# Kernel optimization log

Measured on AMD Instinct MI355X. Metric: run time of the kernel, lower is better.

Reference implementation:

```python
import jax, jax.numpy as jnp
import numpy as np

EPS = 1e-5

def layer_norm(x, g, b):
    mu = jnp.mean(x, axis=-1, keepdims=True)
    var = jnp.var(x, axis=-1, keepdims=True)
    return (x - mu) * jax.lax.rsqrt(var + EPS) * g + b

def setup_inputs() -> dict:
    key = jax.random.key(0)
    ks = jax.random.split(key, 8)
    B, N, C, H = 4, 1024, 1024, 16
    Dh = C * 4
    std = 0.02
    return {
        "x": jax.random.normal(ks[0], (B, N, C), dtype=jnp.float32),
        "qkv_w": jax.random.normal(ks[1], (3 * C, C), dtype=jnp.float32) * std,
        "proj_w": jax.random.normal(ks[2], (C, C), dtype=jnp.float32) * std,
        "proj_b": jnp.zeros((C,), dtype=jnp.float32),
        "fc1_w": jax.random.normal(ks[3], (Dh, C), dtype=jnp.float32) * std,
        "fc1_b": jnp.zeros((Dh,), dtype=jnp.float32),
        "fc2_w": jax.random.normal(ks[4], (C, Dh), dtype=jnp.float32) * std,
        "fc2_b": jnp.zeros((C,), dtype=jnp.float32),
        "ln1_g": jnp.ones((C,), dtype=jnp.float32),
        "ln1_b": jnp.zeros((C,), dtype=jnp.float32),
        "ln2_g": jnp.ones((C,), dtype=jnp.float32),
        "ln2_b": jnp.zeros((C,), dtype=jnp.float32),
        "lnh_g": jnp.ones((Dh,), dtype=jnp.float32),
        "lnh_b": jnp.zeros((Dh,), dtype=jnp.float32),
    }

def reference(x, qkv_w, proj_w, proj_b, fc1_w, fc1_b, fc2_w, fc2_b,
              ln1_g, ln1_b, ln2_g, ln2_b, lnh_g, lnh_b):
    B, N, C = x.shape
    H = 16
    Dh = C // H
    scale = Dh ** (-0.5)

    # --- attention sublayer (pre-norm) ---
    h = layer_norm(x, ln1_g, ln1_b)
    qkv = (h @ qkv_w.T).reshape(B, N, 3, H, Dh).transpose(2, 0, 3, 1, 4)  # [3,B,H,N,Dh]
    q, k, v = qkv[0], qkv[1], qkv[2]
    attn = jnp.einsum('bhid,bhjd->bhij', q, k) * scale
    attn = jax.nn.softmax(attn, axis=-1)
    o = jnp.einsum('bhij,bhjd->bhid', attn, v)          # [B,H,N,Dh]
    o = o.transpose(0, 2, 1, 3).reshape(B, N, C)
    o = o @ proj_w.T + proj_b
    x = x + o

    # --- MLP sublayer (pre-norm, with LN on hidden per use_ln=True) ---
    h = layer_norm(x, ln2_g, ln2_b)
    u = jax.nn.gelu(h @ fc1_w.T + fc1_b, approximate=False)  # torch nn.GELU = erf form
    u = layer_norm(u, lnh_g, lnh_b)
    m = u @ fc2_w.T + fc2_b
    return x + m
```

## Files before the change

### kernel.cpp

```cpp
#include <hip/hip_runtime.h>
#include <hip/hip_bf16.h>
#include <math.h>


#define TOKENS 4096
#define CDIM   1024
#define HEADS  16
#define DHEAD  64
#define HID    4096

typedef __attribute__((ext_vector_type(4))) float  floatx4;
typedef __attribute__((ext_vector_type(8))) short  short8;

__global__ __launch_bounds__(256) void cvt_all(
    const float* __restrict__ s0, const float* __restrict__ s1,
    const float* __restrict__ s2, const float* __restrict__ s3,
    __hip_bfloat16* __restrict__ dst)
{
    long i = (long)blockIdx.x * 256 + threadIdx.x;
    const float* src;
    long base;
    if (i < 768l * 1024)       { src = s0; base = 0; }
    else if (i < 1792l * 1024) { src = s1; base = 768l * 1024; }
    else if (i < 2816l * 1024) { src = s2; base = 1792l * 1024; }
    else                       { src = s3; base = 2816l * 1024; }
    float4 v = ((const float4*)src)[i - base];
    __hip_bfloat16 t[4];
    t[0] = __float2bfloat16(v.x);
    t[1] = __float2bfloat16(v.y);
    t[2] = __float2bfloat16(v.z);
    t[3] = __float2bfloat16(v.w);
    *(uint2*)(dst + 4l * i) = *(uint2*)t;
}

__global__ __launch_bounds__(256) void ln_f32_kernel(
    const float* __restrict__ x, const float* __restrict__ g,
    const float* __restrict__ b, __hip_bfloat16* __restrict__ y, int C)
{
    int row = blockIdx.x;
    const float* xr = x + (long)row * C;
    __hip_bfloat16* yr = y + (long)row * C;

    float s = 0.f, ss = 0.f;
    for (int i = threadIdx.x; i < C; i += 256) {
        float v = xr[i];
        s += v; ss += v * v;
    }
    #pragma unroll
    for (int d = 32; d; d >>= 1) {
        s  += __shfl_down(s, d);
        ss += __shfl_down(ss, d);
    }
    __shared__ float buf[4][2];
    int wid = threadIdx.x >> 6, lane = threadIdx.x & 63;
    if (lane == 0) { buf[wid][0] = s; buf[wid][1] = ss; }
    __syncthreads();
    if (threadIdx.x == 0) {
        s = buf[0][0] + buf[1][0] + buf[2][0] + buf[3][0];
        ss = buf[0][1] + buf[1][1] + buf[2][1] + buf[3][1];
        buf[0][0] = s; buf[0][1] = ss;
    }
    __syncthreads();
    s = buf[0][0]; ss = buf[0][1];

    float invC = 1.f / (float)C;
    float mu = s * invC;
    float var = ss * invC - mu * mu;
    float inv = rsqrtf(var + 1e-5f);
    for (int i = threadIdx.x; i < C; i += 256) {
        yr[i] = __float2bfloat16((xr[i] - mu) * inv * g[i] + b[i]);
    }
}

__global__ __launch_bounds__(256) void ln_bf16_kernel(
    const __hip_bfloat16* __restrict__ x, const float* __restrict__ g,
    const float* __restrict__ b, __hip_bfloat16* __restrict__ y, int C)
{
    int row = blockIdx.x;
    const __hip_bfloat16* xr = x + (long)row * C;
    __hip_bfloat16* yr = y + (long)row * C;

    float s = 0.f, ss = 0.f;
    for (int i = threadIdx.x; i < C; i += 256) {
        float v = __bfloat162float(xr[i]);
        s += v; ss += v * v;
    }
    #pragma unroll
    for (int d = 32; d; d >>= 1) {
        s  += __shfl_down(s, d);
        ss += __shfl_down(ss, d);
    }
    __shared__ float buf[4][2];
    int wid = threadIdx.x >> 6, lane = threadIdx.x & 63;
    if (lane == 0) { buf[wid][0] = s; buf[wid][1] = ss; }
    __syncthreads();
    if (threadIdx.x == 0) {
        s = buf[0][0] + buf[1][0] + buf[2][0] + buf[3][0];
        ss = buf[0][1] + buf[1][1] + buf[2][1] + buf[3][1];
        buf[0][0] = s; buf[0][1] = ss;
    }
    __syncthreads();
    s = buf[0][0]; ss = buf[0][1];

    float invC = 1.f / (float)C;
    float mu = s * invC;
    float var = ss * invC - mu * mu;
    float inv = rsqrtf(var + 1e-5f);
    for (int i = threadIdx.x; i < C; i += 256) {
        float v = __bfloat162float(xr[i]);
        yr[i] = __float2bfloat16((v - mu) * inv * g[i] + b[i]);
    }
}

template <int TN>
__global__ __launch_bounds__(256, 3) void gemm_mfma(
    const __hip_bfloat16* __restrict__ A,
    const __hip_bfloat16* __restrict__ W,
    const float* __restrict__ bias, const float* __restrict__ residual,
    void* __restrict__ Cout, int M, int N, int K, int act, int out_bf16)
{
    constexpr int WN = (TN == 128) ? 2 : 1;
    constexpr int WM = 4 / WN;
    constexpr int FJ = 4;
    constexpr int FI = 128 / (WM * 16);

    __shared__ __hip_bfloat16 Asl[2][128 * 32];
    __shared__ __hip_bfloat16 Bsl[2][TN * 32];

    int tid = threadIdx.x;
    int wave = tid >> 6, lane = tid & 63;

    int mt, nt;
    {
        int gx = gridDim.x, gy = gridDim.y;
        int lin = blockIdx.y * gx + blockIdx.x;
        if ((gy & 7) == 0) {
            int chunk = gy >> 3;
            int xcd = lin & 7, q = lin >> 3;
            mt = xcd * chunk + (q % chunk);
            nt = q / chunk;
        } else { mt = blockIdx.y; nt = blockIdx.x; }
    }
    int bm = mt * 128, bn = nt * TN;
    int wm = wave & (WM - 1), wn = wave / WM;
    int fm = lane & 15, quad = lane >> 4;

    int srow = lane >> 2;
    int skk  = (lane & 3) * 8;

    const __hip_bfloat16* Ap = A + (long)(bm + wave * 16 + srow) * K + skk;
    const __hip_bfloat16* Bp = W + (long)(bn + wave * 16 + srow) * K + skk;
    const long a64 = (long)64 * K;

    const int nk = K / 32;
    floatx4 acc[FI][FJ] = {};
    const int aoff = (wave * 16 + srow) * 32 + skk;

    uint4 a0A, a1A, b0A, b1A;
    uint4 a0B, a1B, b0B, b1B;

#define GLOADA(t) { const long o = (long)(t) * 32; \
    a0A = *(const uint4*)(Ap + o); a1A = *(const uint4*)(Ap + a64 + o); \
    b0A = *(const uint4*)(Bp + o); if (TN == 128) b1A = *(const uint4*)(Bp + a64 + o); }
#define GLOADB(t) { const long o = (long)(t) * 32; \
    a0B = *(const uint4*)(Ap + o); a1B = *(const uint4*)(Ap + a64 + o); \
    b0B = *(const uint4*)(Bp + o); if (TN == 128) b1B = *(const uint4*)(Bp + a64 + o); }
#define LWRITEA(bf) { *(uint4*)&Asl[bf][aoff] = a0A; *(uint4*)&Asl[bf][aoff + 2048] = a1A; \
    *(uint4*)&Bsl[bf][aoff] = b0A; if (TN == 128) *(uint4*)&Bsl[bf][aoff + 2048] = b1A; }
#define LWRITEB(bf) { *(uint4*)&Asl[bf][aoff] = a0B; *(uint4*)&Asl[bf][aoff + 2048] = a1B; \
    *(uint4*)&Bsl[bf][aoff] = b0B; if (TN == 128) *(uint4*)&Bsl[bf][aoff + 2048] = b1B; }

    auto compute = [&](int buf) {
        const __hip_bfloat16* Ab = Asl[buf];
        const __hip_bfloat16* Bb = Bsl[buf];
        short8 bfr[FJ];
        #pragma unroll
        for (int j = 0; j < FJ; ++j)
            bfr[j] = *(const short8*)(Bb + (wn * 64 + j * 16 + fm) * 32 + quad * 8);
        #pragma unroll
        for (int i = 0; i < FI; ++i) {
            short8 af = *(const short8*)(Ab + (wm * FI * 16 + i * 16 + fm) * 32 + quad * 8);
            #pragma unroll
            for (int j = 0; j < FJ; ++j)
                acc[i][j] = __builtin_amdgcn_mfma_f32_16x16x32_bf16(
                    af, bfr[j], acc[i][j], 0, 0, 0);
        }
    };

    GLOADA(0); GLOADB(1);
    LWRITEA(0);
    GLOADA(2);
    __syncthreads();

    for (int kt = 0; kt < nk; kt += 2) {
        compute(0);
        LWRITEB(1);
        if (kt + 3 < nk) GLOADB(kt + 3);
        __syncthreads();
        compute(1);
        if (kt + 2 < nk) {
            LWRITEA(0);
            if (kt + 4 < nk) GLOADA(kt + 4);
        }
        __syncthreads();
    }
#undef GLOADA
#undef GLOADB
#undef LWRITEA
#undef LWRITEB

    int mbase = bm + wm * FI * 16;
    int nbase = bn + wn * 64;
    #pragma unroll
    for (int i = 0; i < FI; ++i) {
        #pragma unroll
        for (int j = 0; j < FJ; ++j) {
            int ncol = nbase + j * 16 + fm;
            #pragma unroll
            for (int r = 0; r < 4; ++r) {
                int mrow = mbase + i * 16 + quad * 4 + r;
                float v = acc[i][j][r];
                if (bias) v += bias[ncol];
                if (act == 1) v = 0.5f * v * (1.f + erff(v * 0.70710678118654752f));
                if (residual) v += residual[(long)mrow * N + ncol];
                if (out_bf16)
                    ((__hip_bfloat16*)Cout)[(long)mrow * N + ncol] = __float2bfloat16(v);
                else
                    ((float*)Cout)[(long)mrow * N + ncol] = v;
            }
        }
    }
}

__global__ __launch_bounds__(256) void attn_mfma(
    const __hip_bfloat16* __restrict__ qkv, __hip_bfloat16* __restrict__ o_out)
{
    __shared__ __align__(16) char Ks[2][64 * 144];
    __shared__ __align__(16) char Vt[2][64 * 144];
    __shared__ __align__(16) char Ps[4 * 16 * 144];

    const int C3 = 3 * CDIM;
    int lin = blockIdx.x;
    int xcd = lin & 7, q = lin >> 3;
    int bh = xcd * 8 + (q >> 4);
    int qt = q & 15;
    int b = bh >> 4, hh = bh & 15;
    int tid = threadIdx.x, wave = tid >> 6, lane = tid & 63;
    int l = lane & 15, quad = lane >> 4;

    const __hip_bfloat16* qrow =
        qkv + (long)(b * 1024 + qt * 64 + wave * 16 + l) * C3 + hh * DHEAD;
    short8 qf0 = *(const short8*)(qrow + quad * 8);
    short8 qf1 = *(const short8*)(qrow + 32 + quad * 8);

    char* Psw = Ps + wave * (16 * 144);

    int sc = tid & 7;
    int skl = tid >> 3;

    const __hip_bfloat16* Kbase = qkv + (long)(b * 1024) * C3 + CDIM + hh * DHEAD;
    const __hip_bfloat16* Vbase = qkv + (long)(b * 1024) * C3 + 2 * CDIM + hh * DHEAD;
    const int kpp = skl ^ (sc << 2);

    floatx4 facc[4] = {};
    float mrun = -1e30f, lrun = 0.f;

    uint4 kA0, kA1, vA0, vA1;
    uint4 kB0, kB1, vB0, vB1;

#define GKV(t, k0, k1, v0, v1) { \
    const __hip_bfloat16* Kg = Kbase + (long)((t) * 64) * C3; \
    const __hip_bfloat16* Vg = Vbase + (long)((t) * 64) * C3; \
    k0 = *(const uint4*)(Kg + (long)skl * C3 + sc * 8); \
    k1 = *(const uint4*)(Kg + (long)(skl + 32) * C3 + sc * 8); \
    v0 = *(const uint4*)(Vg + (long)(2 * skl) * C3 + sc * 8); \
    v1 = *(const uint4*)(Vg + (long)(2 * skl + 1) * C3 + sc * 8); }
#define WKV(bf, k0, k1, v0, v1) { \
    *(uint4*)(Ks[bf] + skl * 144 + sc * 16) = k0; \
    *(uint4*)(Ks[bf] + (skl + 32) * 144 + sc * 16) = k1; \
    const ushort* e0 = (const ushort*)&v0; \
    const ushort* e1 = (const ushort*)&v1; \
    _Pragma("unroll") \
    for (int j = 0; j < 8; ++j) { \
        unsigned dw = (unsigned)e0[j] | ((unsigned)e1[j] << 16); \
        *(unsigned*)(Vt[bf] + (sc * 8 + j) * 144 + kpp * 4) = dw; \
    } }

    auto compute = [&](int buf) {
        floatx4 st[4] = {};
        #pragma unroll
        for (int kb = 0; kb < 4; ++kb) {
            short8 k0 = *(const short8*)(Ks[buf] + (kb * 16 + l) * 144 + quad * 16);
            short8 k1 = *(const short8*)(Ks[buf] + (kb * 16 + l) * 144 + 64 + quad * 16);
            st[kb] = __builtin_amdgcn_mfma_f32_16x16x32_bf16(k0, qf0, st[kb], 0, 0, 0);
            st[kb] = __builtin_amdgcn_mfma_f32_16x16x32_bf16(k1, qf1, st[kb], 0, 0, 0);
        }
        float p[16];
        float tm = -1e30f;
        #pragma unroll
        for (int kb = 0; kb < 4; ++kb)
            #pragma unroll
            for (int r = 0; r < 4; ++r) {
                float s = st[kb][r] * 0.125f;
                p[kb * 4 + r] = s;
                tm = fmaxf(tm, s);
            }
        tm = fmaxf(tm, __shfl_xor(tm, 16));
        tm = fmaxf(tm, __shfl_xor(tm, 32));
        float mn = fmaxf(mrun, tm);
        float alpha = __expf(mrun - mn);
        float psum = 0.f;
        #pragma unroll
        for (int i = 0; i < 16; ++i) { p[i] = __expf(p[i] - mn); psum += p[i]; }
        psum += __shfl_xor(psum, 16);
        psum += __shfl_xor(psum, 32);
        lrun = lrun * alpha + psum;
        mrun = mn;

        #pragma unroll
        for (int kb = 0; kb < 4; ++kb) {
            __hip_bfloat16 t[4];
            #pragma unroll
            for (int r = 0; r < 4; ++r) t[r] = __float2bfloat16(p[kb * 4 + r]);
            *(uint2*)(Psw + l * 144 + kb * 32 + quad * 8) = *(const uint2*)t;
        }

        float a0 = __shfl(alpha, quad * 4 + 0);
        float a1 = __shfl(alpha, quad * 4 + 1);
        float a2 = __shfl(alpha, quad * 4 + 2);
        float a3 = __shfl(alpha, quad * 4 + 3);
        #pragma unroll
        for (int db = 0; db < 4; ++db) {
            facc[db][0] *= a0; facc[db][1] *= a1;
            facc[db][2] *= a2; facc[db][3] *= a3;
        }

        short8 pf0 = *(const short8*)(Psw + l * 144 + quad * 16);
        short8 pf1 = *(const short8*)(Psw + l * 144 + 64 + quad * 16);
        #pragma unroll
        for (int db = 0; db < 4; ++db) {
            int d = db * 16 + l;
            int o3 = (d >> 3) & 7;
            short8 v0 = *(const short8*)(Vt[buf] + d * 144 + ((quad ^ o3) << 4));
            short8 v1 = *(const short8*)(Vt[buf] + d * 144 + (((4 + quad) ^ o3) << 4));
            facc[db] = __builtin_amdgcn_mfma_f32_16x16x32_bf16(pf0, v0, facc[db], 0, 0, 0);
            facc[db] = __builtin_amdgcn_mfma_f32_16x16x32_bf16(pf1, v1, facc[db], 0, 0, 0);
        }
    };

    GKV(0, kA0, kA1, vA0, vA1);
    #pragma unroll 1
    for (int kt = 0; kt < 16; kt += 2) {
        WKV(0, kA0, kA1, vA0, vA1);
        __syncthreads();
        GKV(kt + 1, kB0, kB1, vB0, vB1);
        compute(0);
        WKV(1, kB0, kB1, vB0, vB1);
        __syncthreads();
        if (kt + 2 < 16) GKV(kt + 2, kA0, kA1, vA0, vA1);
        compute(1);
    }
#undef GKV
#undef WKV

    float il0 = 1.f / __shfl(lrun, quad * 4 + 0);
    float il1 = 1.f / __shfl(lrun, quad * 4 + 1);
    float il2 = 1.f / __shfl(lrun, quad * 4 + 2);
    float il3 = 1.f / __shfl(lrun, quad * 4 + 3);
    __hip_bfloat16* orow =
        o_out + (long)(b * 1024 + qt * 64 + wave * 16) * CDIM + hh * DHEAD;
    #pragma unroll
    for (int db = 0; db < 4; ++db) {
        int col = db * 16 + l;
        orow[(quad * 4 + 0) * CDIM + col] = __float2bfloat16(facc[db][0] * il0);
        orow[(quad * 4 + 1) * CDIM + col] = __float2bfloat16(facc[db][1] * il1);
        orow[(quad * 4 + 2) * CDIM + col] = __float2bfloat16(facc[db][2] * il2);
        orow[(quad * 4 + 3) * CDIM + col] = __float2bfloat16(facc[db][3] * il3);
    }
}

extern "C" void kernel_launch(void* const* d_in, const int* in_sizes, int n_in,
                              void* d_out, int out_size, void* d_ws, size_t ws_size,
                              hipStream_t stream)
{
    const float* x      = (const float*)d_in[0];
    const float* qkv_w  = (const float*)d_in[1];
    const float* proj_w = (const float*)d_in[2];
    const float* proj_b = (const float*)d_in[3];
    const float* fc1_w  = (const float*)d_in[4];
    const float* fc1_b  = (const float*)d_in[5];
    const float* fc2_w  = (const float*)d_in[6];
    const float* fc2_b  = (const float*)d_in[7];
    const float* ln1_g  = (const float*)d_in[8];
    const float* ln1_b  = (const float*)d_in[9];
    const float* ln2_g  = (const float*)d_in[10];
    const float* ln2_b  = (const float*)d_in[11];
    const float* lnh_g  = (const float*)d_in[12];
    const float* lnh_b  = (const float*)d_in[13];

    float* out = (float*)d_out;

    __hip_bfloat16* wsb     = (__hip_bfloat16*)d_ws;
    __hip_bfloat16* qkvw_bf = wsb;
    __hip_bfloat16* fc1w_bf = qkvw_bf + 3l * 1024 * 1024;
    __hip_bfloat16* fc2w_bf = fc1w_bf + 4l * 1024 * 1024;
    __hip_bfloat16* projw_bf= fc2w_bf + 4l * 1024 * 1024;
    __hip_bfloat16* h_bf    = projw_bf + 1l * 1024 * 1024;
    __hip_bfloat16* qkv_bf  = h_bf + 4l * 1024 * 1024;
    __hip_bfloat16* o_bf    = qkv_bf + 12l * 1024 * 1024;
    __hip_bfloat16* u_bf    = o_bf + 4l * 1024 * 1024;

    cvt_all<<<12288, 256, 0, stream>>>(qkv_w, fc1_w, fc2_w, proj_w, qkvw_bf);

    ln_f32_kernel<<<TOKENS, 256, 0, stream>>>(x, ln1_g, ln1_b, h_bf, CDIM);
    gemm_mfma<128><<<dim3(3072 / 128, TOKENS / 128), 256, 0, stream>>>(
        h_bf, qkvw_bf, nullptr, nullptr, qkv_bf, TOKENS, 3072, CDIM, 0, 1);
    attn_mfma<<<1024, 256, 0, stream>>>(qkv_bf, o_bf);
    gemm_mfma<64><<<dim3(CDIM / 64, TOKENS / 128), 256, 0, stream>>>(
        o_bf, projw_bf, proj_b, x, out, TOKENS, CDIM, CDIM, 0, 0);
    ln_f32_kernel<<<TOKENS, 256, 0, stream>>>(out, ln2_g, ln2_b, h_bf, CDIM);
    gemm_mfma<128><<<dim3(HID / 128, TOKENS / 128), 256, 0, stream>>>(
        h_bf, fc1w_bf, fc1_b, nullptr, u_bf, TOKENS, HID, CDIM, 1, 1);
    ln_bf16_kernel<<<TOKENS, 256, 0, stream>>>(u_bf, lnh_g, lnh_b, u_bf, HID);
    gemm_mfma<64><<<dim3(CDIM / 64, TOKENS / 128), 256, 0, stream>>>(
        u_bf, fc2w_bf, fc2_b, out, out, TOKENS, CDIM, HID, 0, 0);
}
```

Baseline: 420.0 us.

## Vectorize LayerNorm kernels, restructure GEMM to padded single-buffer K=64 tiles, approximate GELU

The two LayerNorm kernels now use float4 and uint4 vector loads and stores instead of scalar accesses. The GEMM moves from a double-buffered K=32 LDS scheme to a single padded LDS buffer (row stride 144 bytes) holding K=64 per step, with register prefetch of the next tile and two syncs per iteration. Padding the row stride is meant to reduce LDS bank conflicts and halve the iteration count. The exact erf GELU is replaced by a tanh-form sigmoid approximation, which changes numerics relative to the erf reference.

```diff
diff --git a/kernel.cpp b/kernel.cpp
--- a/kernel.cpp
+++ b/kernel.cpp
@@ -38,13 +38,15 @@
     const float* __restrict__ b, __hip_bfloat16* __restrict__ y, int C)
 {
     int row = blockIdx.x;
-    const float* xr = x + (long)row * C;
-    __hip_bfloat16* yr = y + (long)row * C;
+    const float4* xr = (const float4*)(x + (long)row * C);
+    uint2* yr = (uint2*)(y + (long)row * C);
+    const int C4 = C >> 2;
 
     float s = 0.f, ss = 0.f;
-    for (int i = threadIdx.x; i < C; i += 256) {
-        float v = xr[i];
-        s += v; ss += v * v;
+    for (int i = threadIdx.x; i < C4; i += 256) {
+        float4 v = xr[i];
+        s  += v.x + v.y + v.z + v.w;
+        ss += v.x * v.x + v.y * v.y + v.z * v.z + v.w * v.w;
     }
     #pragma unroll
     for (int d = 32; d; d >>= 1) {
@@ -67,8 +69,16 @@
     float mu = s * invC;
     float var = ss * invC - mu * mu;
     float inv = rsqrtf(var + 1e-5f);
-    for (int i = threadIdx.x; i < C; i += 256) {
-        yr[i] = __float2bfloat16((xr[i] - mu) * inv * g[i] + b[i]);
+    const float4* gg = (const float4*)g;
+    const float4* bb = (const float4*)b;
+    for (int i = threadIdx.x; i < C4; i += 256) {
+        float4 v = xr[i], gv = gg[i], bv = bb[i];
+        __hip_bfloat16 t[4];
+        t[0] = __float2bfloat16((v.x - mu) * inv * gv.x + bv.x);
+        t[1] = __float2bfloat16((v.y - mu) * inv * gv.y + bv.y);
+        t[2] = __float2bfloat16((v.z - mu) * inv * gv.z + bv.z);
+        t[3] = __float2bfloat16((v.w - mu) * inv * gv.w + bv.w);
+        yr[i] = *(uint2*)t;
     }
 }
 
@@ -77,13 +87,19 @@
     const float* __restrict__ b, __hip_bfloat16* __restrict__ y, int C)
 {
     int row = blockIdx.x;
-    const __hip_bfloat16* xr = x + (long)row * C;
-    __hip_bfloat16* yr = y + (long)row * C;
+    const uint4* xr = (const uint4*)(x + (long)row * C);
+    uint4* yr = (uint4*)(y + (long)row * C);
+    const int C8 = C >> 3;
 
     float s = 0.f, ss = 0.f;
-    for (int i = threadIdx.x; i < C; i += 256) {
-        float v = __bfloat162float(xr[i]);
-        s += v; ss += v * v;
+    for (int i = threadIdx.x; i < C8; i += 256) {
+        uint4 raw = xr[i];
+        const __hip_bfloat16* p = (const __hip_bfloat16*)&raw;
+        #pragma unroll
+        for (int j = 0; j < 8; ++j) {
+            float v = __bfloat162float(p[j]);
+            s += v; ss += v * v;
+        }
     }
     #pragma unroll
     for (int d = 32; d; d >>= 1) {
@@ -106,12 +122,27 @@
     float mu = s * invC;
     float var = ss * invC - mu * mu;
     float inv = rsqrtf(var + 1e-5f);
-    for (int i = threadIdx.x; i < C; i += 256) {
-        float v = __bfloat162float(xr[i]);
-        yr[i] = __float2bfloat16((v - mu) * inv * g[i] + b[i]);
-    }
-}
-
+    const float4* gg = (const float4*)g;
+    const float4* bb = (const float4*)b;
+    for (int i = threadIdx.x; i < C8; i += 256) {
+        uint4 raw = xr[i];
+        const __hip_bfloat16* p = (const __hip_bfloat16*)&raw;
+        float4 g0 = gg[2 * i], g1 = gg[2 * i + 1];
+        float4 b0 = bb[2 * i], b1 = bb[2 * i + 1];
+        __hip_bfloat16 t[8];
+        t[0] = __float2bfloat16((__bfloat162float(p[0]) - mu) * inv * g0.x + b0.x);
+        t[1] = __float2bfloat16((__bfloat162float(p[1]) - mu) * inv * g0.y + b0.y);
+        t[2] = __float2bfloat16((__bfloat162float(p[2]) - mu) * inv * g0.z + b0.z);
+        t[3] = __float2bfloat16((__bfloat162float(p[3]) - mu) * inv * g0.w + b0.w);
+        t[4] = __float2bfloat16((__bfloat162float(p[4]) - mu) * inv * g1.x + b1.x);
+        t[5] = __float2bfloat16((__bfloat162float(p[5]) - mu) * inv * g1.y + b1.y);
+        t[6] = __float2bfloat16((__bfloat162float(p[6]) - mu) * inv * g1.z + b1.z);
+        t[7] = __float2bfloat16((__bfloat162float(p[7]) - mu) * inv * g1.w + b1.w);
+        yr[i] = *(uint4*)t;
+    }
+}
+
+#define LSTR 144
 template <int TN>
 __global__ __launch_bounds__(256, 3) void gemm_mfma(
     const __hip_bfloat16* __restrict__ A,
@@ -123,9 +154,10 @@
     constexpr int WM = 4 / WN;
     constexpr int FJ = 4;
     constexpr int FI = 128 / (WM * 16);
-
-    __shared__ __hip_bfloat16 Asl[2][128 * 32];
-    __shared__ __hip_bfloat16 Bsl[2][TN * 32];
+    constexpr int BCH = (TN == 128) ? 4 : 2;
+
+    __shared__ __align__(16) char Asl[128 * LSTR];
+    __shared__ __align__(16) char Bsl[TN * LSTR];
 
     int tid = threadIdx.x;
     int wave = tid >> 6, lane = tid & 63;
@@ -145,69 +177,69 @@
     int wm = wave & (WM - 1), wn = wave / WM;
     int fm = lane & 15, quad = lane >> 4;
 
-    int srow = lane >> 2;
-    int skk  = (lane & 3) * 8;
-
-    const __hip_bfloat16* Ap = A + (long)(bm + wave * 16 + srow) * K + skk;
-    const __hip_bfloat16* Bp = W + (long)(bn + wave * 16 + srow) * K + skk;
-    const long a64 = (long)64 * K;
-
-    const int nk = K / 32;
+    int r0 = tid >> 3;
+    int col = tid & 7;
+    const __hip_bfloat16* ApG = A + (long)(bm + r0) * K + col * 8;
+    const __hip_bfloat16* BpG = W + (long)(bn + r0) * K + col * 8;
+    const long r32 = (long)32 * K;
+    const int lo = r0 * LSTR + col * 16;
+
+    uint4 ar[4], br[BCH];
+
+    auto gload = [&](int t) {
+        const long o = (long)t * 64;
+        ar[0] = *(const uint4*)(ApG + o);
+        ar[1] = *(const uint4*)(ApG + r32 + o);
+        ar[2] = *(const uint4*)(ApG + 2 * r32 + o);
+        ar[3] = *(const uint4*)(ApG + 3 * r32 + o);
+        br[0] = *(const uint4*)(BpG + o);
+        br[1] = *(const uint4*)(BpG + r32 + o);
+        if (BCH == 4) {
+            br[2] = *(const uint4*)(BpG + 2 * r32 + o);
+            br[3] = *(const uint4*)(BpG + 3 * r32 + o);
+        }
+    };
+    auto lwrite = [&]() {
+        *(uint4*)(Asl + lo)              = ar[0];
+        *(uint4*)(Asl + lo + 32 * LSTR)  = ar[1];
+        *(uint4*)(Asl + lo + 64 * LSTR)  = ar[2];
+        *(uint4*)(Asl + lo + 96 * LSTR)  = ar[3];
+        *(uint4*)(Bsl + lo)              = br[0];
+        *(uint4*)(Bsl + lo + 32 * LSTR)  = br[1];
+        if (BCH == 4) {
+            *(uint4*)(Bsl + lo + 64 * LSTR) = br[2];
+            *(uint4*)(Bsl + lo + 96 * LSTR) = br[3];
+        }
+    };
+
     floatx4 acc[FI][FJ] = {};
-    const int aoff = (wave * 16 + srow) * 32 + skk;
-
-    uint4 a0A, a1A, b0A, b1A;
-    uint4 a0B, a1B, b0B, b1B;
-
-#define GLOADA(t) { const long o = (long)(t) * 32; \
-    a0A = *(const uint4*)(Ap + o); a1A = *(const uint4*)(Ap + a64 + o); \
-    b0A = *(const uint4*)(Bp + o); if (TN == 128) b1A = *(const uint4*)(Bp + a64 + o); }
-#define GLOADB(t) { const long o = (long)(t) * 32; \
-    a0B = *(const uint4*)(Ap + o); a1B = *(const uint4*)(Ap + a64 + o); \
-    b0B = *(const uint4*)(Bp + o); if (TN == 128) b1B = *(const uint4*)(Bp + a64 + o); }
-#define LWRITEA(bf) { *(uint4*)&Asl[bf][aoff] = a0A; *(uint4*)&Asl[bf][aoff + 2048] = a1A; \
-    *(uint4*)&Bsl[bf][aoff] = b0A; if (TN == 128) *(uint4*)&Bsl[bf][aoff + 2048] = b1A; }
-#define LWRITEB(bf) { *(uint4*)&Asl[bf][aoff] = a0B; *(uint4*)&Asl[bf][aoff + 2048] = a1B; \
-    *(uint4*)&Bsl[bf][aoff] = b0B; if (TN == 128) *(uint4*)&Bsl[bf][aoff + 2048] = b1B; }
-
-    auto compute = [&](int buf) {
-        const __hip_bfloat16* Ab = Asl[buf];
-        const __hip_bfloat16* Bb = Bsl[buf];
-        short8 bfr[FJ];
-        #pragma unroll
-        for (int j = 0; j < FJ; ++j)
-            bfr[j] = *(const short8*)(Bb + (wn * 64 + j * 16 + fm) * 32 + quad * 8);
-        #pragma unroll
-        for (int i = 0; i < FI; ++i) {
-            short8 af = *(const short8*)(Ab + (wm * FI * 16 + i * 16 + fm) * 32 + quad * 8);
+    const int nk = K / 64;
+
+    gload(0);
+    for (int t = 0; t < nk; ++t) {
+        __syncthreads();
+        lwrite();
+        __syncthreads();
+        if (t + 1 < nk) gload(t + 1);
+        #pragma unroll
+        for (int kh = 0; kh < 2; ++kh) {
+            short8 bfr[FJ], af[FI];
             #pragma unroll
             for (int j = 0; j < FJ; ++j)
-                acc[i][j] = __builtin_amdgcn_mfma_f32_16x16x32_bf16(
-                    af, bfr[j], acc[i][j], 0, 0, 0);
-        }
-    };
-
-    GLOADA(0); GLOADB(1);
-    LWRITEA(0);
-    GLOADA(2);
-    __syncthreads();
-
-    for (int kt = 0; kt < nk; kt += 2) {
-        compute(0);
-        LWRITEB(1);
-        if (kt + 3 < nk) GLOADB(kt + 3);
-        __syncthreads();
-        compute(1);
-        if (kt + 2 < nk) {
-            LWRITEA(0);
-            if (kt + 4 < nk) GLOADA(kt + 4);
-        }
-        __syncthreads();
-    }
-#undef GLOADA
-#undef GLOADB
-#undef LWRITEA
-#undef LWRITEB
+                bfr[j] = *(const short8*)(Bsl + (wn * 64 + j * 16 + fm) * LSTR
+                                          + kh * 64 + quad * 16);
+            #pragma unroll
+            for (int i = 0; i < FI; ++i)
+                af[i] = *(const short8*)(Asl + (wm * FI * 16 + i * 16 + fm) * LSTR
+                                         + kh * 64 + quad * 16);
+            #pragma unroll
+            for (int i = 0; i < FI; ++i)
+                #pragma unroll
+                for (int j = 0; j < FJ; ++j)
+                    acc[i][j] = __builtin_amdgcn_mfma_f32_16x16x32_bf16(
+                        af[i], bfr[j], acc[i][j], 0, 0, 0);
+        }
+    }
 
     int mbase = bm + wm * FI * 16;
     int nbase = bn + wn * 64;
@@ -221,7 +253,10 @@
                 int mrow = mbase + i * 16 + quad * 4 + r;
                 float v = acc[i][j][r];
                 if (bias) v += bias[ncol];
-                if (act == 1) v = 0.5f * v * (1.f + erff(v * 0.70710678118654752f));
+                if (act == 1) {
+                    float z = v * (1.5957691216f + 0.0713548162f * v * v);
+                    v = v / (1.f + __expf(-z));
+                }
                 if (residual) v += residual[(long)mrow * N + ncol];
                 if (out_bf16)
                     ((__hip_bfloat16*)Cout)[(long)mrow * N + ncol] = __float2bfloat16(v);
```

New measurement: 800.0 us. +90.5%, slower.
